# Optimization experiments

Measured on AMD Instinct MI355X. Metric: run time of the kernel, lower is better.

## Reference

```python
import jax, jax.numpy as jnp
import numpy as np


def _conv(x, w, padding):
    # x: (N,H,W,Cin), w: (kh,kw,Cin,Cout)
    return jax.lax.conv_general_dilated(x, w, (1, 1), padding,
                                        dimension_numbers=('NHWC', 'HWIO', 'NHWC'))


def _hard_sigmoid(x):
    # Keras default recurrent_activation for ConvLSTM2D
    return jnp.clip(0.2 * x + 0.5, 0.0, 1.0)


def _convlstm(x, Wx, Wh, b):
    # x: (B,T,H,W,Cin); Wx: (3,3,Cin,4F) input conv (VALID, as Keras padding default);
    # Wh: (3,3,F,4F) recurrent conv (SAME, Keras always); b: (4F,). Gate order i,f,c,o.
    B, T, H, W, C = x.shape
    F = Wh.shape[2]
    # Input convolutions are state-independent: compute for all timesteps at once.
    xg = _conv(x.reshape(B * T, H, W, C), Wx, 'VALID') + b  # (B*T, H-2, W-2, 4F)
    Ho, Wo = xg.shape[1], xg.shape[2]
    xg = xg.reshape(B, T, Ho, Wo, 4 * F).transpose(1, 0, 2, 3, 4)  # (T,B,Ho,Wo,4F)
    h0 = jnp.zeros((B, Ho, Wo, F), x.dtype)

    def step(carry, g_t):
        h, c = carry
        g = g_t + _conv(h, Wh, 'SAME')
        i, f, cc, o = jnp.split(g, 4, axis=-1)
        c = _hard_sigmoid(f) * c + _hard_sigmoid(i) * jnp.tanh(cc)
        h = _hard_sigmoid(o) * jnp.tanh(c)
        return (h, c), h

    _, hs = jax.lax.scan(step, (h0, h0), xg)  # hs: (T,B,Ho,Wo,F)
    return hs.transpose(1, 0, 2, 3, 4)


def _maxpool_hw(x):
    # MaxPooling3D pool=(1,2,2), stride=pool, padding='same' on (B,T,H,W,C)
    return jax.lax.reduce_window(x, -jnp.inf, jax.lax.max,
                                 (1, 1, 2, 2, 1), (1, 1, 2, 2, 1), 'SAME')


def setup_inputs() -> dict:
    key = jax.random.key(0)
    ks = jax.random.split(key, 11)
    B, T, H, W, C = 32, 24, 128, 128, 3
    NUM_CLASSES = 50
    FLAT = 24 * 7 * 7 * 16  # = 18816, see shape trace
    p = lambda k, s: (jax.random.normal(k, s, jnp.float32) * 0.05)
    return {
        'x': jax.random.normal(ks[0], (B, T, H, W, C), jnp.float32),
        'Wx1': p(ks[1], (3, 3, 3, 16)),  'Wh1': p(ks[2], (3, 3, 4, 16)),  'b1': jnp.zeros((16,), jnp.float32),
        'Wx2': p(ks[3], (3, 3, 4, 32)),  'Wh2': p(ks[4], (3, 3, 8, 32)),  'b2': jnp.zeros((32,), jnp.float32),
        'Wx3': p(ks[5], (3, 3, 8, 48)),  'Wh3': p(ks[6], (3, 3, 12, 48)), 'b3': jnp.zeros((48,), jnp.float32),
        'Wx4': p(ks[7], (3, 3, 12, 64)), 'Wh4': p(ks[8], (3, 3, 16, 64)), 'b4': jnp.zeros((64,), jnp.float32),
        'Wd': p(ks[9], (FLAT, NUM_CLASSES)), 'bd': jnp.zeros((NUM_CLASSES,), jnp.float32),
    }


def reference(x, Wx1, Wh1, b1, Wx2, Wh2, b2, Wx3, Wh3, b3, Wx4, Wh4, b4, Wd, bd):
    # Dropout layers are identity at inference.
    x = _maxpool_hw(_convlstm(x, Wx1, Wh1, b1))
    x = _maxpool_hw(_convlstm(x, Wx2, Wh2, b2))
    x = _maxpool_hw(_convlstm(x, Wx3, Wh3, b3))
    x = _maxpool_hw(_convlstm(x, Wx4, Wh4, b4))
    x = x.reshape(x.shape[0], -1)  # Keras Flatten: row-major over (T,H,W,C)
    return jax.nn.softmax(x @ Wd + bd, axis=-1)
```

## Files before the change

kernel.cpp:

```cpp
#include <hip/hip_runtime.h>
#include <math.h>


static __device__ __forceinline__ float hsig(float x) {
    return fminf(fmaxf(fmaf(0.2f, x, 0.5f), 0.0f), 1.0f);
}
static __device__ __forceinline__ float ftanh(float x) {
    float e = __builtin_amdgcn_exp2f(x * 2.88539008177792681f);
    return 1.0f - 2.0f * __builtin_amdgcn_rcpf(e + 1.0f);
}

constexpr int H1SL = 32 * 126 * 126 * 4;
constexpr int H2SL = 32 * 61 * 61 * 8;
constexpr int H3SL = 32 * 29 * 29 * 12;
constexpr int H4SL = 32 * 13 * 13 * 16;
constexpr size_t O_H1 = 0;
constexpr size_t O_H2 = O_H1 + 2 * (size_t)H1SL;
constexpr size_t O_H3 = O_H2 + 2 * (size_t)H2SL;
constexpr size_t O_H4 = O_H3 + 2 * (size_t)H3SL;
constexpr size_t O_C1 = O_H4 + 2 * (size_t)H4SL;
constexpr size_t O_C2 = O_C1 + (size_t)H1SL;
constexpr size_t O_C3 = O_C2 + (size_t)H2SL;
constexpr size_t O_C4 = O_C3 + (size_t)H3SL;
constexpr size_t O_P1 = O_C4 + (size_t)H4SL;
constexpr size_t O_P2 = O_P1 + (size_t)(768 * 63 * 63 * 4);
constexpr size_t O_P3 = O_P2 + (size_t)(768 * 31 * 31 * 8);
constexpr size_t O_P4 = O_P3 + (size_t)(768 * 15 * 15 * 12);
constexpr size_t O_DP = O_P4 + (size_t)(768 * 7 * 7 * 16);

__host__ __device__ static inline int role_blocks(int r, int s) {
    int t;
    switch (r) {
    case 0: t = s - 6; return (t >= 0 && t < 24) ? 85   : 0;
    case 1: t = s - 4; return (t >= 0 && t < 24) ? 421  : 0;
    case 2: t = s;     return (t >= 0 && t < 24) ? 993  : 0;
    case 3: t = s - 2; return (t >= 0 && t < 24) ? 1861 : 0;
    case 4: t = s - 1; return (t >= 0 && t < 24) ? 497  : 0;
    case 5: t = s - 3; return (t >= 0 && t < 24) ? 121  : 0;
    case 6: t = s - 5; return (t >= 0 && t < 24) ? 29   : 0;
    case 7: t = s - 7; return (t >= 0 && t < 24) ? 7    : 0;
    }
    return 0;
}
constexpr int NSTAGES = 31;

__device__ __forceinline__
void step_pair_d(const float* __restrict__ P,
                 const float* __restrict__ Wx,
                 const float* __restrict__ Wh,
                 const float* __restrict__ bias,
                 const float* __restrict__ h_prev,
                 float* __restrict__ h_cur,
                 float* __restrict__ cbuf,
                 int t, int lb)
{
    constexpr int CIN = 3, F = 4, HIN = 128, WIN = 128;
    constexpr int B = 32, T = 24, HO = 126, WO = 126, G = 16;
    constexpr int XP = WO / 2;
    constexpr int NPAIR = B * HO * XP;
    const int id = lb * 256 + (int)threadIdx.x;
    if (id >= NPAIR) return;
    const int xp = id % XP;
    const int yy = (id / XP) % HO;
    const int b  = id / (XP * HO);
    const int x0 = 2 * xp;

    float acc[2][4][F];
    #pragma unroll
    for (int u = 0; u < 2; ++u)
        #pragma unroll
        for (int g = 0; g < 4; ++g)
            #pragma unroll
            for (int f = 0; f < F; ++f)
                acc[u][g][f] = bias[g * F + f];

    const float* Pt = P + (size_t)(b * T + t) * HIN * WIN * CIN;
    #pragma unroll
    for (int ky = 0; ky < 3; ++ky) {
        const float* prow = Pt + ((size_t)(yy + ky) * WIN + x0) * CIN;
        float pv[4 * CIN];
        #pragma unroll
        for (int j = 0; j < 2 * CIN; ++j) {
            float2 v2 = reinterpret_cast<const float2*>(prow)[j];
            pv[2 * j] = v2.x; pv[2 * j + 1] = v2.y;
        }
        #pragma unroll
        for (int dx = 0; dx < 4; ++dx)
            #pragma unroll
            for (int ci = 0; ci < CIN; ++ci) {
                const float v = pv[dx * CIN + ci];
                #pragma unroll
                for (int u = 0; u < 2; ++u) {
                    const int kx = dx - u;
                    if (kx >= 0 && kx <= 2) {
                        const float* wr =
                            Wx + (size_t)((ky * 3 + kx) * CIN + ci) * G;
                        #pragma unroll
                        for (int g = 0; g < 4; ++g)
                            #pragma unroll
                            for (int f = 0; f < F; ++f)
                                acc[u][g][f] = fmaf(v, wr[g * F + f], acc[u][g][f]);
                    }
                }
            }
    }

    if (t > 0) {
        #pragma unroll
        for (int ky = 0; ky < 3; ++ky) {
            const int hy = yy + ky - 1;
            if (hy < 0 || hy >= HO) continue;
            const float* hrow = h_prev + ((size_t)b * HO + hy) * WO * F;
            #pragma unroll
            for (int dx = 0; dx < 4; ++dx) {
                const int hx = x0 - 1 + dx;
                if (dx == 0 && x0 == 0) continue;
                if (dx == 3 && hx >= WO) continue;
                const float4* h4 =
                    reinterpret_cast<const float4*>(hrow + (size_t)hx * F);
                float hv[F];
                #pragma unroll
                for (int j = 0; j < F / 4; ++j) {
                    float4 v4 = h4[j];
                    hv[4*j] = v4.x; hv[4*j+1] = v4.y;
                    hv[4*j+2] = v4.z; hv[4*j+3] = v4.w;
                }
                #pragma unroll
                for (int ci = 0; ci < F; ++ci) {
                    const float v = hv[ci];
                    #pragma unroll
                    for (int u = 0; u < 2; ++u) {
                        const int kx = dx - u;
                        if (kx >= 0 && kx <= 2) {
                            const float* wr =
                                Wh + (size_t)((ky * 3 + kx) * F + ci) * G;
                            #pragma unroll
                            for (int g = 0; g < 4; ++g)
                                #pragma unroll
                                for (int f = 0; f < F; ++f)
                                    acc[u][g][f] =
                                        fmaf(v, wr[g * F + f], acc[u][g][f]);
                        }
                    }
                }
            }
        }
    }

    #pragma unroll
    for (int u = 0; u < 2; ++u) {
        const size_t pix = ((size_t)b * HO + yy) * WO + (x0 + u);
        float cn[F], ho[F];
        float* cp = cbuf + pix * F;
        #pragma unroll
        for (int j = 0; j < F / 4; ++j) {
            float4 c4 = (t > 0) ? reinterpret_cast<float4*>(cp)[j]
                                : make_float4(0.f, 0.f, 0.f, 0.f);
            float cold[4] = {c4.x, c4.y, c4.z, c4.w};
            #pragma unroll
            for (int v = 0; v < 4; ++v) {
                const int f = 4 * j + v;
                const float ig = hsig(acc[u][0][f]), fg = hsig(acc[u][1][f]);
                const float cc = ftanh(acc[u][2][f]), og = hsig(acc[u][3][f]);
                cn[f] = fmaf(fg, cold[v], ig * cc);
                ho[f] = og * ftanh(cn[f]);
            }
            reinterpret_cast<float4*>(cp)[j] =
                make_float4(cn[4*j], cn[4*j+1], cn[4*j+2], cn[4*j+3]);
        }
        float* hp = h_cur + pix * F;
        #pragma unroll
        for (int j = 0; j < F / 4; ++j)
            reinterpret_cast<float4*>(hp)[j] =
                make_float4(ho[4*j], ho[4*j+1], ho[4*j+2], ho[4*j+3]);
    }
}

template<int CIN, int F, int HIN, int WIN>
__device__ __forceinline__
void step_split_d(const float* __restrict__ P,
                  const float* __restrict__ Wx,
                  const float* __restrict__ Wh,
                  const float* __restrict__ bias,
                  const float* __restrict__ h_prev,
                  float* __restrict__ h_cur,
                  float* __restrict__ cbuf,
                  int t, int lb, float* __restrict__ gb)
{
    constexpr int B = 32, T = 24, HO = HIN - 2, WO = WIN - 2, G = 4 * F;
    constexpr int NPIX = B * HO * WO;
    const int tid = (int)threadIdx.x, lane = tid & 63;
    const int w = __builtin_amdgcn_readfirstlane(tid >> 6);
    const int pix = lb * 64 + lane;
    const int pp  = (pix < NPIX) ? pix : NPIX - 1;
    const int sp  = pp % (HO * WO);
    const int b   = pp / (HO * WO);
    const int xx  = sp % WO, yy = sp / WO;

    float acc[F];
    #pragma unroll
    for (int f = 0; f < F; ++f) acc[f] = bias[w * F + f];

    const float* Pt = P + (size_t)(b * T + t) * HIN * WIN * CIN;
    #pragma unroll
    for (int ky = 0; ky < 3; ++ky) {
        #pragma unroll
        for (int kx = 0; kx < 3; ++kx) {
            const float* prow = Pt + ((size_t)(yy + ky) * WIN + (xx + kx)) * CIN;
            float pv[CIN];
            #pragma unroll
            for (int j = 0; j < CIN / 4; ++j) {
                float4 v4 = reinterpret_cast<const float4*>(prow)[j];
                pv[4*j] = v4.x; pv[4*j+1] = v4.y; pv[4*j+2] = v4.z; pv[4*j+3] = v4.w;
            }
            #pragma unroll
            for (int ci = 0; ci < CIN; ++ci) {
                const float v = pv[ci];
                const float* wr = Wx + (size_t)((ky * 3 + kx) * CIN + ci) * G + w * F;
                #pragma unroll
                for (int f = 0; f < F; ++f)
                    acc[f] = fmaf(v, wr[f], acc[f]);
            }
        }
    }

    if (t > 0) {
        const float* Hp = h_prev + (size_t)b * HO * WO * F;
        #pragma unroll
        for (int ky = 0; ky < 3; ++ky) {
            const int hy = yy + ky - 1;
            if (hy < 0 || hy >= HO) continue;
            #pragma unroll
            for (int kx = 0; kx < 3; ++kx) {
                const int hx = xx + kx - 1;
                if (hx < 0 || hx >= WO) continue;
                const float4* h4 = reinterpret_cast<const float4*>(
                    Hp + ((size_t)hy * WO + hx) * F);
                float hv[F];
                #pragma unroll
                for (int j = 0; j < F / 4; ++j) {
                    float4 v4 = h4[j];
                    hv[4*j] = v4.x; hv[4*j+1] = v4.y; hv[4*j+2] = v4.z; hv[4*j+3] = v4.w;
                }
                #pragma unroll
                for (int ci = 0; ci < F; ++ci) {
                    const float v = hv[ci];
                    const float* wr = Wh + (size_t)((ky * 3 + kx) * F + ci) * G + w * F;
                    #pragma unroll
                    for (int f = 0; f < F; ++f)
                        acc[f] = fmaf(v, wr[f], acc[f]);
                }
            }
        }
    }

    #pragma unroll
    for (int f = 0; f < F; ++f) gb[w * (64 * F) + lane * F + f] = acc[f];
    __syncthreads();

    #pragma unroll
    for (int r2 = 0; r2 < F / 4; ++r2) {
        const int it = r2 * 256 + tid;
        const int pl = it / F, fo = it % F;
        const int pix2 = lb * 64 + pl;
        if (pix2 < NPIX) {
            const float ig = hsig(gb[0 * (64*F) + it]), fg = hsig(gb[1 * (64*F) + it]);
            const float cc = ftanh(gb[2 * (64*F) + it]), og = hsig(gb[3 * (64*F) + it]);
            const size_t cix = (size_t)pix2 * F + fo;
            const float cold = (t > 0) ? cbuf[cix] : 0.0f;
            const float cnw = fmaf(fg, cold, ig * cc);
            cbuf[cix] = cnw;
            const int s2 = pix2 % (HO * WO);
            const int b2 = pix2 / (HO * WO);
            h_cur[((size_t)b2 * HO * WO + s2) * F + fo] = og * ftanh(cnw);
        }
    }
}

template<int C, int H, int W, int HP, int WP>
__device__ __forceinline__
void pool_slice_d(const float* __restrict__ h,
                  float* __restrict__ outF,
                  int t, int lb)
{
    constexpr int B = 32, T = 24;
    const int idx = lb * 256 + (int)threadIdx.x;
    if (idx >= B * HP * WP) return;
    const int xo = idx % WP;
    const int yo = (idx / WP) % HP;
    const int b  = idx / (WP * HP);
    const int y0 = 2 * yo, x0 = 2 * xo;
    const float* p = h + ((size_t)(b * H + y0) * W + x0) * C;
    float m[C];
    #pragma unroll
    for (int j = 0; j < C / 4; ++j) {
        float4 v = reinterpret_cast<const float4*>(p)[j];
        m[4*j] = v.x; m[4*j+1] = v.y; m[4*j+2] = v.z; m[4*j+3] = v.w;
    }
    if (x0 + 1 < W) {
        const float4* q = reinterpret_cast<const float4*>(p + C);
        #pragma unroll
        for (int j = 0; j < C / 4; ++j) {
            float4 v = q[j];
            m[4*j]   = fmaxf(m[4*j],   v.x); m[4*j+1] = fmaxf(m[4*j+1], v.y);
            m[4*j+2] = fmaxf(m[4*j+2], v.z); m[4*j+3] = fmaxf(m[4*j+3], v.w);
        }
    }
    if (y0 + 1 < H) {
        const float4* q = reinterpret_cast<const float4*>(p + (size_t)W * C);
        #pragma unroll
        for (int j = 0; j < C / 4; ++j) {
            float4 v = q[j];
            m[4*j]   = fmaxf(m[4*j],   v.x); m[4*j+1] = fmaxf(m[4*j+1], v.y);
            m[4*j+2] = fmaxf(m[4*j+2], v.z); m[4*j+3] = fmaxf(m[4*j+3], v.w);
        }
        if (x0 + 1 < W) {
            const float4* q2 = reinterpret_cast<const float4*>(p + (size_t)(W + 1) * C);
            #pragma unroll
            for (int j = 0; j < C / 4; ++j) {
                float4 v = q2[j];
                m[4*j]   = fmaxf(m[4*j],   v.x); m[4*j+1] = fmaxf(m[4*j+1], v.y);
                m[4*j+2] = fmaxf(m[4*j+2], v.z); m[4*j+3] = fmaxf(m[4*j+3], v.w);
            }
        }
    }
    float* o = outF + ((size_t)(b * T + t) * HP * WP + (size_t)yo * WP + xo) * C;
    #pragma unroll
    for (int j = 0; j < C / 4; ++j)
        reinterpret_cast<float4*>(o)[j] =
            make_float4(m[4*j], m[4*j+1], m[4*j+2], m[4*j+3]);
}

__global__ __launch_bounds__(256)
void pipe_k(const float* __restrict__ x,
            const float* __restrict__ Wx1, const float* __restrict__ Wh1, const float* __restrict__ b1,
            const float* __restrict__ Wx2, const float* __restrict__ Wh2, const float* __restrict__ b2,
            const float* __restrict__ Wx3, const float* __restrict__ Wh3, const float* __restrict__ b3,
            const float* __restrict__ Wx4, const float* __restrict__ Wh4, const float* __restrict__ b4,
            float* __restrict__ ws, int s)
{
    float* h1 = ws + O_H1;  float* h2 = ws + O_H2;
    float* h3 = ws + O_H3;  float* h4 = ws + O_H4;
    float* c1 = ws + O_C1;  float* c2 = ws + O_C2;
    float* c3 = ws + O_C3;  float* c4 = ws + O_C4;
    float* p1 = ws + O_P1;  float* p2 = ws + O_P2;
    float* p3 = ws + O_P3;  float* p4 = ws + O_P4;

    __shared__ float gb[4 * 64 * 16];

    int bid = (int)blockIdx.x, r = 0, cum = 0;
    for (; r < 8; ++r) {
        int n = role_blocks(r, s);
        if (bid < cum + n) break;
        cum += n;
    }
    const int lb = bid - cum;

    switch (r) {
    case 0: { const int t = s - 6;
        step_split_d<12, 16, 15, 15>(p3, Wx4, Wh4, b4,
            h4 + ((t - 1) & 1) * (size_t)H4SL, h4 + (t & 1) * (size_t)H4SL,
            c4, t, lb, gb); } break;
    case 1: { const int t = s - 4;
        step_split_d<8, 12, 31, 31>(p2, Wx3, Wh3, b3,
            h3 + ((t - 1) & 1) * (size_t)H3SL, h3 + (t & 1) * (size_t)H3SL,
            c3, t, lb, gb); } break;
    case 2: { const int t = s;
        step_pair_d(x, Wx1, Wh1, b1,
            h1 + ((t - 1) & 1) * (size_t)H1SL, h1 + (t & 1) * (size_t)H1SL,
            c1, t, lb); } break;
    case 3: { const int t = s - 2;
        step_split_d<4, 8, 63, 63>(p1, Wx2, Wh2, b2,
            h2 + ((t - 1) & 1) * (size_t)H2SL, h2 + (t & 1) * (size_t)H2SL,
            c2, t, lb, gb); } break;
    case 4: { const int t = s - 1;
        pool_slice_d<4, 126, 126, 63, 63>(h1 + (t & 1) * (size_t)H1SL, p1, t, lb); } break;
    case 5: { const int t = s - 3;
        pool_slice_d<8, 61, 61, 31, 31>(h2 + (t & 1) * (size_t)H2SL, p2, t, lb); } break;
    case 6: { const int t = s - 5;
        pool_slice_d<12, 29, 29, 15, 15>(h3 + (t & 1) * (size_t)H3SL, p3, t, lb); } break;
    case 7: { const int t = s - 7;
        pool_slice_d<16, 13, 13, 7, 7>(h4 + (t & 1) * (size_t)H4SL, p4, t, lb); } break;
    }
}

__global__ __launch_bounds__(256)
void dense_partial_k(const float* __restrict__ X, const float* __restrict__ Wd,
                     float* __restrict__ part)
{
    constexpr int FLAT = 18816, K = 50, NC = 12, CHUNK = FLAT / NC;
    const int b = blockIdx.x, ch = blockIdx.y;
    const int tid = threadIdx.x, lane = tid & 63, wv = tid >> 6;
    const float* xp = X + (size_t)b * FLAT;
    const int i0 = ch * CHUNK + wv * (CHUNK / 4);
    float a0 = 0.f, a1 = 0.f, a2 = 0.f, a3 = 0.f;
    if (lane < K) {
        for (int i = i0; i < i0 + CHUNK / 4; i += 4) {
            a0 = fmaf(xp[i + 0], Wd[(size_t)(i + 0) * K + lane], a0);
            a1 = fmaf(xp[i + 1], Wd[(size_t)(i + 1) * K + lane], a1);
            a2 = fmaf(xp[i + 2], Wd[(size_t)(i + 2) * K + lane], a2);
            a3 = fmaf(xp[i + 3], Wd[(size_t)(i + 3) * K + lane], a3);
        }
    }
    __shared__ float red[256];
    red[tid] = (a0 + a1) + (a2 + a3);
    __syncthreads();
    if (tid < 64 && lane < K)
        part[((size_t)b * NC + ch) * K + lane]
            = red[tid] + red[tid + 64] + red[tid + 128] + red[tid + 192];
}

__global__ __launch_bounds__(64)
void dense_finish_k(const float* __restrict__ part, const float* __restrict__ bd,
                    float* __restrict__ out)
{
    constexpr int K = 50, NC = 12;
    const int b = blockIdx.x, lane = threadIdx.x;
    float v = -INFINITY;
    if (lane < K) {
        v = bd[lane];
        #pragma unroll
        for (int c = 0; c < NC; ++c)
            v += part[((size_t)b * NC + c) * K + lane];
    }
    float m = v;
    #pragma unroll
    for (int off = 32; off > 0; off >>= 1) m = fmaxf(m, __shfl_xor(m, off));
    float e = (lane < K) ? __expf(v - m) : 0.0f;
    float sgm = e;
    #pragma unroll
    for (int off = 32; off > 0; off >>= 1) sgm += __shfl_xor(sgm, off);
    if (lane < K) out[(size_t)b * K + lane] = e / sgm;
}

extern "C" void kernel_launch(void* const* d_in, const int* in_sizes, int n_in,
                              void* d_out, int out_size, void* d_ws, size_t ws_size,
                              hipStream_t stream)
{
    const float* x   = (const float*)d_in[0];
    const float* Wx1 = (const float*)d_in[1];
    const float* Wh1 = (const float*)d_in[2];
    const float* b1  = (const float*)d_in[3];
    const float* Wx2 = (const float*)d_in[4];
    const float* Wh2 = (const float*)d_in[5];
    const float* b2  = (const float*)d_in[6];
    const float* Wx3 = (const float*)d_in[7];
    const float* Wh3 = (const float*)d_in[8];
    const float* b3  = (const float*)d_in[9];
    const float* Wx4 = (const float*)d_in[10];
    const float* Wh4 = (const float*)d_in[11];
    const float* b4  = (const float*)d_in[12];
    const float* Wd  = (const float*)d_in[13];
    const float* bd  = (const float*)d_in[14];
    float* out = (float*)d_out;
    float* ws  = (float*)d_ws;

    for (int s = 0; s < NSTAGES; ++s) {
        int nb = 0;
        for (int r = 0; r < 8; ++r) nb += role_blocks(r, s);
        pipe_k<<<nb, 256, 0, stream>>>(x,
                                       Wx1, Wh1, b1, Wx2, Wh2, b2,
                                       Wx3, Wh3, b3, Wx4, Wh4, b4,
                                       ws, s);
    }

    dense_partial_k<<<dim3(32, 12), 256, 0, stream>>>(ws + O_P4, Wd, ws + O_DP);
    dense_finish_k<<<32, 64, 0, stream>>>(ws + O_DP, bd, out);
}
```

Before: 1.189 ms.

## Fuse maxpool into next layer's input conv and fold dense into pipeline

Removes the separate pooling roles for layers 1-3. Each next ConvLSTM layer now computes 2x2 max-pooled inputs on the fly from the previous layer's hidden state, which eliminates the pooled intermediate buffers and shortens the pipeline from 31 to 29 stages. Layer 2 switches to a one-thread-per-pixel merged-gate kernel without shared memory. The dense partial products are interleaved into the stage launches, which removes one kernel launch. The cost is redundant pooling reads (each pooled value is re-read up to 9 times per conv window) and tighter launch bounds that may pressure registers.

```diff
diff --git a/kernel.cpp b/kernel.cpp
--- a/kernel.cpp
+++ b/kernel.cpp
@@ -22,27 +22,64 @@
 constexpr size_t O_C2 = O_C1 + (size_t)H1SL;
 constexpr size_t O_C3 = O_C2 + (size_t)H2SL;
 constexpr size_t O_C4 = O_C3 + (size_t)H3SL;
-constexpr size_t O_P1 = O_C4 + (size_t)H4SL;
-constexpr size_t O_P2 = O_P1 + (size_t)(768 * 63 * 63 * 4);
-constexpr size_t O_P3 = O_P2 + (size_t)(768 * 31 * 31 * 8);
-constexpr size_t O_P4 = O_P3 + (size_t)(768 * 15 * 15 * 12);
+constexpr size_t O_P4 = O_C4 + (size_t)H4SL;
 constexpr size_t O_DP = O_P4 + (size_t)(768 * 7 * 7 * 16);
 
 __host__ __device__ static inline int role_blocks(int r, int s) {
     int t;
     switch (r) {
-    case 0: t = s - 6; return (t >= 0 && t < 24) ? 85   : 0;
-    case 1: t = s - 4; return (t >= 0 && t < 24) ? 421  : 0;
+    case 0: t = s - 3; return (t >= 0 && t < 24) ? 85   : 0;
+    case 1: t = s - 2; return (t >= 0 && t < 24) ? 421  : 0;
     case 2: t = s;     return (t >= 0 && t < 24) ? 993  : 0;
-    case 3: t = s - 2; return (t >= 0 && t < 24) ? 1861 : 0;
-    case 4: t = s - 1; return (t >= 0 && t < 24) ? 497  : 0;
-    case 5: t = s - 3; return (t >= 0 && t < 24) ? 121  : 0;
-    case 6: t = s - 5; return (t >= 0 && t < 24) ? 29   : 0;
-    case 7: t = s - 7; return (t >= 0 && t < 24) ? 7    : 0;
+    case 3: t = s - 1; return (t >= 0 && t < 24) ? 466  : 0;
+    case 4: t = s - 4; return (t >= 0 && t < 24) ? 7    : 0;
+    case 5: return (s >= 6 && s <= 28 && ((s - 6) & 1) == 0) ? 32 : 0;
     }
     return 0;
 }
-constexpr int NSTAGES = 31;
+constexpr int NSTAGES = 29;
+
+template<int C, int H, int W>
+__device__ __forceinline__
+void pooled_read(const float* __restrict__ hsl, int b, int py, int px,
+                 float out[C])
+{
+    const float* p = hsl + ((size_t)(b * H + 2 * py) * W + 2 * px) * C;
+    #pragma unroll
+    for (int j = 0; j < C / 4; ++j) {
+        float4 v = reinterpret_cast<const float4*>(p)[j];
+        out[4*j] = v.x; out[4*j+1] = v.y; out[4*j+2] = v.z; out[4*j+3] = v.w;
+    }
+    const bool xv = (W % 2 == 0) || (2 * px + 1 < W);
+    const bool yv = (H % 2 == 0) || (2 * py + 1 < H);
+    if (xv) {
+        const float4* q = reinterpret_cast<const float4*>(p + C);
+        #pragma unroll
+        for (int j = 0; j < C / 4; ++j) {
+            float4 v = q[j];
+            out[4*j]   = fmaxf(out[4*j],   v.x); out[4*j+1] = fmaxf(out[4*j+1], v.y);
+            out[4*j+2] = fmaxf(out[4*j+2], v.z); out[4*j+3] = fmaxf(out[4*j+3], v.w);
+        }
+    }
+    if (yv) {
+        const float4* q = reinterpret_cast<const float4*>(p + (size_t)W * C);
+        #pragma unroll
+        for (int j = 0; j < C / 4; ++j) {
+            float4 v = q[j];
+            out[4*j]   = fmaxf(out[4*j],   v.x); out[4*j+1] = fmaxf(out[4*j+1], v.y);
+            out[4*j+2] = fmaxf(out[4*j+2], v.z); out[4*j+3] = fmaxf(out[4*j+3], v.w);
+        }
+        if (xv) {
+            const float4* q2 = reinterpret_cast<const float4*>(p + (size_t)(W + 1) * C);
+            #pragma unroll
+            for (int j = 0; j < C / 4; ++j) {
+                float4 v = q2[j];
+                out[4*j]   = fmaxf(out[4*j],   v.x); out[4*j+1] = fmaxf(out[4*j+1], v.y);
+                out[4*j+2] = fmaxf(out[4*j+2], v.z); out[4*j+3] = fmaxf(out[4*j+3], v.w);
+            }
+        }
+    }
+}
 
 __device__ __forceinline__
 void step_pair_d(const float* __restrict__ P,
@@ -176,18 +213,119 @@
     }
 }
 
-template<int CIN, int F, int HIN, int WIN>
+template<int CP, int F, int HR, int WR>
 __device__ __forceinline__
-void step_split_d(const float* __restrict__ P,
-                  const float* __restrict__ Wx,
-                  const float* __restrict__ Wh,
-                  const float* __restrict__ bias,
-                  const float* __restrict__ h_prev,
-                  float* __restrict__ h_cur,
-                  float* __restrict__ cbuf,
-                  int t, int lb, float* __restrict__ gb)
-{
-    constexpr int B = 32, T = 24, HO = HIN - 2, WO = WIN - 2, G = 4 * F;
+void step_merged_pool_d(const float* __restrict__ hin,
+                        const float* __restrict__ Wx,
+                        const float* __restrict__ Wh,
+                        const float* __restrict__ bias,
+                        const float* __restrict__ h_prev,
+                        float* __restrict__ h_cur,
+                        float* __restrict__ cbuf,
+                        int t, int lb)
+{
+    constexpr int B = 32;
+    constexpr int HP = (HR + 1) / 2, WP = (WR + 1) / 2;
+    constexpr int HO = HP - 2, WO = WP - 2, G = 4 * F;
+    constexpr int NPIX = B * HO * WO;
+    const int pix = lb * 256 + (int)threadIdx.x;
+    if (pix >= NPIX) return;
+    const int xx = pix % WO;
+    const int yy = (pix / WO) % HO;
+    const int b  = pix / (WO * HO);
+
+    float acc[4][F];
+    #pragma unroll
+    for (int g = 0; g < 4; ++g)
+        #pragma unroll
+        for (int f = 0; f < F; ++f)
+            acc[g][f] = bias[g * F + f];
+
+    #pragma unroll
+    for (int ky = 0; ky < 3; ++ky)
+        #pragma unroll
+        for (int kx = 0; kx < 3; ++kx) {
+            float pv[CP];
+            pooled_read<CP, HR, WR>(hin, b, yy + ky, xx + kx, pv);
+            #pragma unroll
+            for (int ci = 0; ci < CP; ++ci) {
+                const float v = pv[ci];
+                const float* wr = Wx + (size_t)((ky * 3 + kx) * CP + ci) * G;
+                #pragma unroll
+                for (int g = 0; g < 4; ++g)
+                    #pragma unroll
+                    for (int f = 0; f < F; ++f)
+                        acc[g][f] = fmaf(v, wr[g * F + f], acc[g][f]);
+            }
+        }
+
+    if (t > 0) {
+        #pragma unroll
+        for (int ky = 0; ky < 3; ++ky) {
+            const int hy = yy + ky - 1;
+            if (hy < 0 || hy >= HO) continue;
+            #pragma unroll
+            for (int kx = 0; kx < 3; ++kx) {
+                const int hx = xx + kx - 1;
+                if (hx < 0 || hx >= WO) continue;
+                const float4* h4 = reinterpret_cast<const float4*>(
+                    h_prev + (((size_t)b * HO + hy) * WO + hx) * F);
+                float hv[F];
+                #pragma unroll
+                for (int j = 0; j < F / 4; ++j) {
+                    float4 v4 = h4[j];
+                    hv[4*j] = v4.x; hv[4*j+1] = v4.y; hv[4*j+2] = v4.z; hv[4*j+3] = v4.w;
+                }
+                #pragma unroll
+                for (int ci = 0; ci < F; ++ci) {
+                    const float v = hv[ci];
+                    const float* wr = Wh + (size_t)((ky * 3 + kx) * F + ci) * G;
+                    #pragma unroll
+                    for (int g = 0; g < 4; ++g)
+                        #pragma unroll
+                        for (int f = 0; f < F; ++f)
+                            acc[g][f] = fmaf(v, wr[g * F + f], acc[g][f]);
+                }
+            }
+        }
+    }
+
+    const size_t base = (size_t)pix * F;
+    float* cp = cbuf + base;
+    float* hp = h_cur + base;
+    #pragma unroll
+    for (int j = 0; j < F / 4; ++j) {
+        float4 c4 = (t > 0) ? reinterpret_cast<float4*>(cp)[j]
+                            : make_float4(0.f, 0.f, 0.f, 0.f);
+        float cold[4] = {c4.x, c4.y, c4.z, c4.w};
+        float cn[4], ho[4];
+        #pragma unroll
+        for (int v = 0; v < 4; ++v) {
+            const int f = 4 * j + v;
+            const float ig = hsig(acc[0][f]), fg = hsig(acc[1][f]);
+            const float cc = ftanh(acc[2][f]), og = hsig(acc[3][f]);
+            cn[v] = fmaf(fg, cold[v], ig * cc);
+            ho[v] = og * ftanh(cn[v]);
+        }
+        reinterpret_cast<float4*>(cp)[j] = make_float4(cn[0], cn[1], cn[2], cn[3]);
+        reinterpret_cast<float4*>(hp)[j] = make_float4(ho[0], ho[1], ho[2], ho[3]);
+    }
+}
+
+template<int CP, int F, int HR, int WR>
+__device__ __forceinline__
+void step_split_pool_d(const float* __restrict__ hin,
+                       const float* __restrict__ Wx,
+                       const float* __restrict__ Wh,
+                       const float* __restrict__ bias,
+                       const float* __restrict__ h_prev,
+                       float* __restrict__ h_cur,
+                       float* __restrict__ cbuf,
+                       int t, int lb, float* __restrict__ gb)
+{
+    constexpr int B = 32;
+    constexpr int HP = (HR + 1) / 2, WP = (WR + 1) / 2;
+    constexpr int HO = HP - 2, WO = WP - 2, G = 4 * F;
     constexpr int NPIX = B * HO * WO;
     const int tid = (int)threadIdx.x, lane = tid & 63;
     const int w = __builtin_amdgcn_readfirstlane(tid >> 6);
@@ -201,28 +339,21 @@
     #pragma unroll
     for (int f = 0; f < F; ++f) acc[f] = bias[w * F + f];
 
-    const float* Pt = P + (size_t)(b * T + t) * HIN * WIN * CIN;
-    #pragma unroll
-    for (int ky = 0; ky < 3; ++ky) {
+    #pragma unroll
+    for (int ky = 0; ky < 3; ++ky)
         #pragma unroll
         for (int kx = 0; kx < 3; ++kx) {
-            const float* prow = Pt + ((size_t)(yy + ky) * WIN + (xx + kx)) * CIN;
-            float pv[CIN];
-            #pragma unroll
-            for (int j = 0; j < CIN / 4; ++j) {
-                float4 v4 = reinterpret_cast<const float4*>(prow)[j];
-                pv[4*j] = v4.x; pv[4*j+1] = v4.y; pv[4*j+2] = v4.z; pv[4*j+3] = v4.w;
-            }
-            #pragma unroll
-            for (int ci = 0; ci < CIN; ++ci) {
+            float pv[CP];
+            pooled_read<CP, HR, WR>(hin, b, yy + ky, xx + kx, pv);
+            #pragma unroll
+            for (int ci = 0; ci < CP; ++ci) {
                 const float v = pv[ci];
-                const float* wr = Wx + (size_t)((ky * 3 + kx) * CIN + ci) * G + w * F;
+                const float* wr = Wx + (size_t)((ky * 3 + kx) * CP + ci) * G + w * F;
                 #pragma unroll
                 for (int f = 0; f < F; ++f)
                     acc[f] = fmaf(v, wr[f], acc[f]);
             }
         }
-    }
 
     if (t > 0) {
         const float* Hp = h_prev + (size_t)b * HO * WO * F;
@@ -270,60 +401,23 @@
             const float cold = (t > 0) ? cbuf[cix] : 0.0f;
             const float cnw = fmaf(fg, cold, ig * cc);
             cbuf[cix] = cnw;
-            const int s2 = pix2 % (HO * WO);
-            const int b2 = pix2 / (HO * WO);
-            h_cur[((size_t)b2 * HO * WO + s2) * F + fo] = og * ftanh(cnw);
-        }
-    }
-}
-
-template<int C, int H, int W, int HP, int WP>
+            h_cur[cix] = og * ftanh(cnw);
+        }
+    }
+}
+
 __device__ __forceinline__
-void pool_slice_d(const float* __restrict__ h,
-                  float* __restrict__ outF,
-                  int t, int lb)
-{
-    constexpr int B = 32, T = 24;
+void pool4_slice_d(const float* __restrict__ h, float* __restrict__ outF,
+                   int t, int lb)
+{
+    constexpr int B = 32, T = 24, C = 16, H = 13, W = 13, HP = 7, WP = 7;
     const int idx = lb * 256 + (int)threadIdx.x;
     if (idx >= B * HP * WP) return;
     const int xo = idx % WP;
     const int yo = (idx / WP) % HP;
     const int b  = idx / (WP * HP);
-    const int y0 = 2 * yo, x0 = 2 * xo;
-    const float* p = h + ((size_t)(b * H + y0) * W + x0) * C;
     float m[C];
-    #pragma unroll
-    for (int j = 0; j < C / 4; ++j) {
-        float4 v = reinterpret_cast<const float4*>(p)[j];
-        m[4*j] = v.x; m[4*j+1] = v.y; m[4*j+2] = v.z; m[4*j+3] = v.w;
-    }
-    if (x0 + 1 < W) {
-        const float4* q = reinterpret_cast<const float4*>(p + C);
-        #pragma unroll
-        for (int j = 0; j < C / 4; ++j) {
-            float4 v = q[j];
-            m[4*j]   = fmaxf(m[4*j],   v.x); m[4*j+1] = fmaxf(m[4*j+1], v.y);
-            m[4*j+2] = fmaxf(m[4*j+2], v.z); m[4*j+3] = fmaxf(m[4*j+3], v.w);
-        }
-    }
-    if (y0 + 1 < H) {
-        const float4* q = reinterpret_cast<const float4*>(p + (size_t)W * C);
-        #pragma unroll
-        for (int j = 0; j < C / 4; ++j) {
-            float4 v = q[j];
-            m[4*j]   = fmaxf(m[4*j],   v.x); m[4*j+1] = fmaxf(m[4*j+1], v.y);
-            m[4*j+2] = fmaxf(m[4*j+2], v.z); m[4*j+3] = fmaxf(m[4*j+3], v.w);
-        }
-        if (x0 + 1 < W) {
-            const float4* q2 = reinterpret_cast<const float4*>(p + (size_t)(W + 1) * C);
-            #pragma unroll
-            for (int j = 0; j < C / 4; ++j) {
-                float4 v = q2[j];
-                m[4*j]   = fmaxf(m[4*j],   v.x); m[4*j+1] = fmaxf(m[4*j+1], v.y);
-                m[4*j+2] = fmaxf(m[4*j+2], v.z); m[4*j+3] = fmaxf(m[4*j+3], v.w);
-            }
-        }
-    }
+    pooled_read<C, H, W>(h, b, yo, xo, m);
     float* o = outF + ((size_t)(b * T + t) * HP * WP + (size_t)yo * WP + xo) * C;
     #pragma unroll
     for (int j = 0; j < C / 4; ++j)
@@ -331,66 +425,14 @@
             make_float4(m[4*j], m[4*j+1], m[4*j+2], m[4*j+3]);
 }
 
-__global__ __launch_bounds__(256)
-void pipe_k(const float* __restrict__ x,
-            const float* __restrict__ Wx1, const float* __restrict__ Wh1, const float* __restrict__ b1,
-            const float* __restrict__ Wx2, const float* __restrict__ Wh2, const float* __restrict__ b2,
-            const float* __restrict__ Wx3, const float* __restrict__ Wh3, const float* __restrict__ b3,
-            const float* __restrict__ Wx4, const float* __restrict__ Wh4, const float* __restrict__ b4,
-            float* __restrict__ ws, int s)
-{
-    float* h1 = ws + O_H1;  float* h2 = ws + O_H2;
-    float* h3 = ws + O_H3;  float* h4 = ws + O_H4;
-    float* c1 = ws + O_C1;  float* c2 = ws + O_C2;
-    float* c3 = ws + O_C3;  float* c4 = ws + O_C4;
-    float* p1 = ws + O_P1;  float* p2 = ws + O_P2;
-    float* p3 = ws + O_P3;  float* p4 = ws + O_P4;
-
-    __shared__ float gb[4 * 64 * 16];
-
-    int bid = (int)blockIdx.x, r = 0, cum = 0;
-    for (; r < 8; ++r) {
-        int n = role_blocks(r, s);
-        if (bid < cum + n) break;
-        cum += n;
-    }
-    const int lb = bid - cum;
-
-    switch (r) {
-    case 0: { const int t = s - 6;
-        step_split_d<12, 16, 15, 15>(p3, Wx4, Wh4, b4,
-            h4 + ((t - 1) & 1) * (size_t)H4SL, h4 + (t & 1) * (size_t)H4SL,
-            c4, t, lb, gb); } break;
-    case 1: { const int t = s - 4;
-        step_split_d<8, 12, 31, 31>(p2, Wx3, Wh3, b3,
-            h3 + ((t - 1) & 1) * (size_t)H3SL, h3 + (t & 1) * (size_t)H3SL,
-            c3, t, lb, gb); } break;
-    case 2: { const int t = s;
-        step_pair_d(x, Wx1, Wh1, b1,
-            h1 + ((t - 1) & 1) * (size_t)H1SL, h1 + (t & 1) * (size_t)H1SL,
-            c1, t, lb); } break;
-    case 3: { const int t = s - 2;
-        step_split_d<4, 8, 63, 63>(p1, Wx2, Wh2, b2,
-            h2 + ((t - 1) & 1) * (size_t)H2SL, h2 + (t & 1) * (size_t)H2SL,
-            c2, t, lb, gb); } break;
-    case 4: { const int t = s - 1;
-        pool_slice_d<4, 126, 126, 63, 63>(h1 + (t & 1) * (size_t)H1SL, p1, t, lb); } break;
-    case 5: { const int t = s - 3;
-        pool_slice_d<8, 61, 61, 31, 31>(h2 + (t & 1) * (size_t)H2SL, p2, t, lb); } break;
-    case 6: { const int t = s - 5;
-        pool_slice_d<12, 29, 29, 15, 15>(h3 + (t & 1) * (size_t)H3SL, p3, t, lb); } break;
-    case 7: { const int t = s - 7;
-        pool_slice_d<16, 13, 13, 7, 7>(h4 + (t & 1) * (size_t)H4SL, p4, t, lb); } break;
-    }
-}
-
-__global__ __launch_bounds__(256)
-void dense_partial_k(const float* __restrict__ X, const float* __restrict__ Wd,
-                     float* __restrict__ part)
+__device__ __forceinline__
+void dense_partial_d(const float* __restrict__ X, const float* __restrict__ Wd,
+                     float* __restrict__ part, int ch, int lb,
+                     float* __restrict__ red)
 {
     constexpr int FLAT = 18816, K = 50, NC = 12, CHUNK = FLAT / NC;
-    const int b = blockIdx.x, ch = blockIdx.y;
-    const int tid = threadIdx.x, lane = tid & 63, wv = tid >> 6;
+    const int b = lb;
+    const int tid = (int)threadIdx.x, lane = tid & 63, wv = tid >> 6;
     const float* xp = X + (size_t)b * FLAT;
     const int i0 = ch * CHUNK + wv * (CHUNK / 4);
     float a0 = 0.f, a1 = 0.f, a2 = 0.f, a3 = 0.f;
@@ -402,12 +444,63 @@
             a3 = fmaf(xp[i + 3], Wd[(size_t)(i + 3) * K + lane], a3);
         }
     }
-    __shared__ float red[256];
     red[tid] = (a0 + a1) + (a2 + a3);
     __syncthreads();
     if (tid < 64 && lane < K)
         part[((size_t)b * NC + ch) * K + lane]
             = red[tid] + red[tid + 64] + red[tid + 128] + red[tid + 192];
+}
+
+__global__ __launch_bounds__(256, 4)
+void pipe_k(const float* __restrict__ x,
+            const float* __restrict__ Wx1, const float* __restrict__ Wh1, const float* __restrict__ b1,
+            const float* __restrict__ Wx2, const float* __restrict__ Wh2, const float* __restrict__ b2,
+            const float* __restrict__ Wx3, const float* __restrict__ Wh3, const float* __restrict__ b3,
+            const float* __restrict__ Wx4, const float* __restrict__ Wh4, const float* __restrict__ b4,
+            const float* __restrict__ Wd,
+            float* __restrict__ ws, int s)
+{
+    float* h1 = ws + O_H1;  float* h2 = ws + O_H2;
+    float* h3 = ws + O_H3;  float* h4 = ws + O_H4;
+    float* c1 = ws + O_C1;  float* c2 = ws + O_C2;
+    float* c3 = ws + O_C3;  float* c4 = ws + O_C4;
+    float* p4 = ws + O_P4;  float* dp = ws + O_DP;
+
+    __shared__ float gb[4 * 64 * 16];
+
+    int bid = (int)blockIdx.x, r = 0, cum = 0;
+    for (; r < 6; ++r) {
+        int n = role_blocks(r, s);
+        if (bid < cum + n) break;
+        cum += n;
+    }
+    const int lb = bid - cum;
+
+    switch (r) {
+    case 0: { const int t = s - 3;
+        step_split_pool_d<12, 16, 29, 29>(h3 + (t & 1) * (size_t)H3SL,
+            Wx4, Wh4, b4,
+            h4 + ((t - 1) & 1) * (size_t)H4SL, h4 + (t & 1) * (size_t)H4SL,
+            c4, t, lb, gb); } break;
+    case 1: { const int t = s - 2;
+        step_split_pool_d<8, 12, 61, 61>(h2 + (t & 1) * (size_t)H2SL,
+            Wx3, Wh3, b3,
+            h3 + ((t - 1) & 1) * (size_t)H3SL, h3 + (t & 1) * (size_t)H3SL,
+            c3, t, lb, gb); } break;
+    case 2: { const int t = s;
+        step_pair_d(x, Wx1, Wh1, b1,
+            h1 + ((t - 1) & 1) * (size_t)H1SL, h1 + (t & 1) * (size_t)H1SL,
+            c1, t, lb); } break;
+    case 3: { const int t = s - 1;
+        step_merged_pool_d<4, 8, 126, 126>(h1 + (t & 1) * (size_t)H1SL,
+            Wx2, Wh2, b2,
+            h2 + ((t - 1) & 1) * (size_t)H2SL, h2 + (t & 1) * (size_t)H2SL,
+            c2, t, lb); } break;
+    case 4: { const int t = s - 4;
+        pool4_slice_d(h4 + (t & 1) * (size_t)H4SL, p4, t, lb); } break;
+    case 5: { const int ch = (s - 6) >> 1;
+        dense_partial_d(p4, Wd, dp, ch, lb, gb); } break;
+    }
 }
 
 __global__ __launch_bounds__(64)
@@ -457,13 +550,11 @@
 
     for (int s = 0; s < NSTAGES; ++s) {
         int nb = 0;
-        for (int r = 0; r < 8; ++r) nb += role_blocks(r, s);
+        for (int r = 0; r < 6; ++r) nb += role_blocks(r, s);
         pipe_k<<<nb, 256, 0, stream>>>(x,
                                        Wx1, Wh1, b1, Wx2, Wh2, b2,
                                        Wx3, Wh3, b3, Wx4, Wh4, b4,
-                                       ws, s);
-    }
-
-    dense_partial_k<<<dim3(32, 12), 256, 0, stream>>>(ws + O_P4, Wd, ws + O_DP);
+                                       Wd, ws, s);
+    }
     dense_finish_k<<<32, 64, 0, stream>>>(ws + O_DP, bd, out);
 }
```

Result: slower. 2.583 ms (+117.3%).
